# Kernel optimization log

Hardware: AMD Instinct MI355X
Metric: run time of the kernel (lower is better)

The kernel has to match this reference:

```python
import jax, jax.numpy as jnp
import numpy as np

N_CHAINS = 4
CHAIN_LEN = 512
N = N_CHAINS * CHAIN_LEN          # 2048 residues
H = 128                           # h_channels
FC = 3                            # frame_channels
CIN = H + FC                      # fused sphere channels (131)
NH = 8                            # attention heads
VD = H // 4                       # attn value channels per head
NCOEF = 4                         # lmax=1 -> (lmax+1)^2 coefficients
KNN_K = 30
LR_K = 10
NEG = jnp.float32(-1e30)

BB_IDEAL = np.array([[-0.525, 1.363, 0.0], [0.0, 0.0, 0.0], [1.526, 0.0, 0.0]], np.float32)  # N, CA, C ideal coords


def _safe_norm(v, keepdims=False):
    return jnp.sqrt(jnp.sum(v * v, axis=-1, keepdims=keepdims) + 1e-12)


def _normalize(v):
    return v / _safe_norm(v, keepdims=True)


def _edge_rot_mat(vec):
    # deterministic orthonormal frame with first row along the edge direction
    x = _normalize(vec)
    ref = jnp.where(jnp.abs(x[..., :1]) > 0.99,
                    jnp.array([0.0, 1.0, 0.0], x.dtype),
                    jnp.array([1.0, 0.0, 0.0], x.dtype))
    z = _normalize(jnp.cross(x, ref))
    y = jnp.cross(z, x)
    return jnp.stack([x, y, z], axis=-2)          # [E,3,3]


def _rbf(d, d_min=0.0, d_max=20.0, n=16):
    mu = jnp.linspace(d_min, d_max, n)
    sigma = (d_max - d_min) / n
    return jnp.exp(-(((d[..., None] - mu) / sigma) ** 2))


def _relpos(edge_index, n=16):
    d = (edge_index[0] - edge_index[1]).astype(jnp.float32)
    freq = jnp.exp(jnp.arange(0, n, 2, dtype=jnp.float32) * (-np.log(10000.0) / n))
    ang = d[:, None] * freq
    return jnp.concatenate([jnp.cos(ang), jnp.sin(ang)], axis=-1)


def _quat_to_rot(q):
    w, x, y, z = q[..., 0], q[..., 1], q[..., 2], q[..., 3]
    r0 = jnp.stack([1 - 2 * (y * y + z * z), 2 * (x * y - w * z), 2 * (x * z + w * y)], -1)
    r1 = jnp.stack([2 * (x * y + w * z), 1 - 2 * (x * x + z * z), 2 * (y * z - w * x)], -1)
    r2 = jnp.stack([2 * (x * z - w * y), 2 * (y * z + w * x), 1 - 2 * (x * x + y * y)], -1)
    return jnp.stack([r0, r1, r2], -2)


def _build_edges(trans, batch, seq_local_edge_index):
    d2 = jnp.sum((trans[:, None] - trans[None]) ** 2, -1)   # [N,N]
    same = batch[:, None] == batch[None]
    eye = jnp.eye(N, dtype=bool)
    d2m = jnp.where(same & ~eye, d2, jnp.float32(1e30))
    _, knn_idx = jax.lax.top_k(-d2m, KNN_K)                 # kNN neighbors
    g = jax.random.gumbel(jax.random.key(42), d2m.shape)
    _, lr_idx = jax.lax.top_k(-1.5 * jnp.log(d2m) + g, LR_K)  # inv-cubic sampling p ~ d^-3
    src = jnp.concatenate([knn_idx.reshape(-1), lr_idx.reshape(-1), seq_local_edge_index[0]])
    dst = jnp.concatenate([jnp.repeat(jnp.arange(N), KNN_K), jnp.repeat(jnp.arange(N), LR_K), seq_local_edge_index[1]])
    return jnp.stack([src, dst])


def _forward(rots, trans, node_features, Wa1, ba1, Wa2, Wv, Wo, Wg, Wf1, Wf2, Wr1, br1, Wr2, br2, Wr3, br3, Wt, batch, x_mask, noising_mask, seq_local_edge_index):
    edge_index = _build_edges(trans, batch, seq_local_edge_index)
    src, dst = edge_index[0], edge_index[1]
    vec = trans[src] - trans[dst]
    dist = _safe_norm(vec)
    valid = jnp.isfinite(dist) & (dist > 1e-3)              # edge_select mask (kept static-shape)
    R = _edge_rot_mat(vec)                                  # [E,3,3] per-edge Wigner (l=1)
    ef = jnp.concatenate([_rbf(dist), _relpos(edge_index)], -1)  # [E,32]
    # fuse node embedding with backbone frame atoms and editability flag
    bb_atoms = jnp.einsum('nij,aj->nai', rots, jnp.asarray(BB_IDEAL)) + trans[:, None]  # [N,3atoms,3]
    fused = jnp.zeros((N, NCOEF, CIN), node_features.dtype)
    fused = fused.at[:, :, :H].set(node_features)
    fused = fused.at[:, 1:4, H:].set(jnp.swapaxes(bb_atoms, -1, -2))
    editable = noising_mask & (~x_mask)
    fused = fused.at[:, 0, -1].set(editable.astype(fused.dtype))
    # SO3-equivariant attention (TransBlockV2)
    x0 = fused[:, 0]                                        # invariant l=0 features [N,CIN]
    a_in = jnp.concatenate([x0[src], x0[dst], ef], -1)      # [E, 2*CIN+32]
    logits = jax.nn.leaky_relu(a_in @ Wa1 + ba1) @ Wa2      # [E,NH]
    logits = jnp.where(valid[:, None], logits, NEG)
    m = jax.ops.segment_max(logits, dst, num_segments=N)
    m = jnp.where(m > NEG / 2, m, 0.0)
    p = jnp.where(valid[:, None], jnp.exp(logits - m[dst]), 0.0)
    z = jax.ops.segment_sum(p, dst, num_segments=N)
    attn = p / (z[dst] + 1e-9)                              # segment softmax over incoming edges
    xs = fused[src]
    xs = xs.at[:, 1:4].set(jnp.einsum('eij,ejc->eic', R, xs[:, 1:4]))  # rotate l=1 into edge frame
    v = (xs @ Wv).reshape(xs.shape[0], NCOEF, NH, VD)
    msg = (attn[:, None, :, None] * v).reshape(xs.shape[0], NCOEF, NH * VD)
    msg = msg.at[:, 1:4].set(jnp.einsum('eji,ejc->eic', R, msg[:, 1:4]))  # rotate back (R^T)
    agg = jax.ops.segment_sum(msg, dst, num_segments=N)     # [N,4,NH*VD]
    out = agg @ Wo                                          # [N,4,H]
    # gated equivariant FFN
    y0 = out[:, 0]
    gate = jax.nn.sigmoid(y0 @ Wg)
    f0 = jax.nn.relu(y0 @ Wf1) @ Wf2
    bb_update = jnp.concatenate([(y0 + f0)[:, None], out[:, 1:4] * gate[:, None, :]], axis=1)
    # frame rotation update from invariants
    inv = bb_update[:, 0]
    h1 = jax.nn.relu(inv @ Wr1 + br1)
    h2 = jax.nn.relu(h1 @ Wr2 + br2)
    qv = (h2 @ Wr3 + br3)[:, :3]
    quat = jnp.concatenate([jnp.ones_like(qv[:, :1]), qv], -1)
    quat = quat / jnp.linalg.norm(quat, axis=-1, keepdims=True)
    rot_update = _quat_to_rot(quat)
    # equivariant translation update (SO3_LinearV2 on l=1)
    trans_update = (bb_update[:, 1:4] @ Wt)[..., 0]         # [N,3]
    rots_new = jnp.where(noising_mask[:, None, None], jnp.einsum('nij,njk->nik', rots, rot_update), rots)
    trans_new = jnp.where(noising_mask[:, None], trans + trans_update, trans)
    return rots_new, trans_new, bb_update


def setup_inputs():
    key = jax.random.key(0)
    ks = jax.random.split(key, 20)
    q = jax.random.normal(ks[0], (N, 4))
    q = q / jnp.linalg.norm(q, axis=-1, keepdims=True)
    rots = _quat_to_rot(q)                                  # proper rotation matrices
    trans = jax.random.normal(ks[1], (N, 3)) * 10.0
    node_features = jax.random.normal(ks[2], (N, NCOEF, H)) * 0.1
    batch = jnp.repeat(jnp.arange(N_CHAINS), CHAIN_LEN)
    x_mask = jax.random.bernoulli(ks[3], 0.1, (N,))
    noising_mask = jax.random.bernoulli(ks[4], 0.5, (N,))
    idx = jnp.arange(N)
    nxt = jnp.where((idx + 1) % CHAIN_LEN == 0, idx, idx + 1)
    seq_local_edge_index = jnp.stack([jnp.concatenate([idx, nxt]), jnp.concatenate([nxt, idx])])

    def lin(k, i, o):
        return jax.random.normal(k, (i, o)) / np.sqrt(i)

    AIN = 2 * CIN + 32
    return dict(
        rots=rots, trans=trans, node_features=node_features,
        Wa1=lin(ks[5], AIN, H), ba1=jnp.zeros((H,)),
        Wa2=lin(ks[6], H, NH),
        Wv=lin(ks[7], CIN, NH * VD),
        Wo=lin(ks[8], NH * VD, H),
        Wg=lin(ks[9], H, H), Wf1=lin(ks[10], H, H), Wf2=lin(ks[11], H, H),
        Wr1=lin(ks[12], H, 2 * H), br1=jnp.zeros((2 * H,)),
        Wr2=lin(ks[13], 2 * H, H), br2=jnp.zeros((H,)),
        Wr3=lin(ks[14], H, 6), br3=jnp.zeros((6,)),
        Wt=lin(ks[15], H, 1),
        batch=batch, x_mask=x_mask, noising_mask=noising_mask,
        seq_local_edge_index=seq_local_edge_index)


def reference(rots, trans, node_features, Wa1, ba1, Wa2, Wv, Wo, Wg, Wf1, Wf2, Wr1, br1, Wr2, br2, Wr3, br3, Wt, batch, x_mask, noising_mask, seq_local_edge_index):
    return _forward(rots, trans, node_features, Wa1, ba1, Wa2, Wv, Wo, Wg, Wf1, Wf2, Wr1, br1, Wr2, br2, Wr3, br3, Wt, batch, x_mask, noising_mask, seq_local_edge_index)
```

## Files before the change

### kernel.cpp

```cpp
#include <hip/hip_runtime.h>
#include <hip/hip_bf16.h>
#include <math.h>

#define NN 2048
#define CHAIN 512
#define KNN 30
#define LRK 10
#define NFIX 40
#define NSLOT 42
#define HPAD 132
#define AGPAD 260
#define NREL 1023

#define OUT_ROT 0
#define OUT_TRANS (NN*9)
#define OUT_BB (NN*9 + NN*3)

#define THREEFRY_PARTITIONABLE 1

__device__ __forceinline__ int xcd_swz(int b){ return ((b & 7) << 8) | (b >> 3); }

__device__ __forceinline__ unsigned rotl32(unsigned x, unsigned r){ return (x<<r)|(x>>(32u-r)); }

__device__ __forceinline__ void tf_block(unsigned &x0, unsigned &x1){
  const unsigned k0 = 0u, k1 = 42u, k2 = 0x1BD11BDAu ^ 0u ^ 42u;
  x0 += k0; x1 += k1;
#define TFR(a) x0 += x1; x1 = rotl32(x1,(a)); x1 ^= x0;
  TFR(13) TFR(15) TFR(26) TFR(6)   x0 += k1; x1 += k2 + 1u;
  TFR(17) TFR(29) TFR(16) TFR(24)  x0 += k2; x1 += k0 + 2u;
  TFR(13) TFR(15) TFR(26) TFR(6)   x0 += k0; x1 += k1 + 3u;
  TFR(17) TFR(29) TFR(16) TFR(24)  x0 += k1; x1 += k2 + 4u;
  TFR(13) TFR(15) TFR(26) TFR(6)   x0 += k2; x1 += k0 + 5u;
#undef TFR
}

__device__ __forceinline__ float gumbel_from_bits(unsigned bits){
  float f = __uint_as_float((bits >> 9) | 0x3f800000u) - 1.0f;
  const float tiny = 1.17549435e-38f;
  float u = fmaxf(tiny, f * (1.0f - tiny) + tiny);
  return -logf(-logf(u));
}

__device__ __forceinline__ float gumbel_at(unsigned p){
#if THREEFRY_PARTITIONABLE
  unsigned x0 = 0u, x1 = p;
  tf_block(x0, x1);
  return gumbel_from_bits(x0 ^ x1);
#else
  const unsigned HALF = (NN*(unsigned)NN)/2u;
  unsigned c0, c1; bool lo = p < HALF;
  if(lo){ c0 = p; c1 = p + HALF; } else { c0 = p - HALF; c1 = p; }
  tf_block(c0, c1);
  return gumbel_from_bits(lo ? c0 : c1);
#endif
}

__global__ __launch_bounds__(256) void k_pretop(
    const float* __restrict__ rots, const float* __restrict__ trans,
    const float* __restrict__ nf, const float* __restrict__ Wa1,
    const float* __restrict__ Wv, const int* __restrict__ xmask,
    const int* __restrict__ nmask,
    float* __restrict__ P, float* __restrict__ U, float* __restrict__ V,
    int* __restrict__ srcs, float* __restrict__ Trel)
{
  __shared__ __align__(16) char smem[4*4*132*4];
  int bb = blockIdx.x, t = threadIdx.x;

  if(bb >= NN + 512){
    int r = (bb - (NN+512))*2 + (t >> 7);
    int k = t & 127;
    if(r < NREL){
      float rel = (float)(r - 511);
      float acc = 0.f;
#pragma unroll
      for(int j=0;j<8;j++){
        float fr = expf((float)(2*j) * (float)(-0.5756462732485115));
        float ang = rel * fr;
        acc += cosf(ang) * Wa1[(278+j)*128 + k];
        acc += sinf(ang) * Wa1[(286+j)*128 + k];
      }
      Trel[r*128 + k] = acc;
    }
    return;
  }

  if(bb < NN){
    unsigned* s_kk = (unsigned*)smem;
    unsigned* s_lk = s_kk + CHAIN;
    int i = bb;
    int base = (i >> 9) << 9;
    float tx = trans[i*3+0], ty = trans[i*3+1], tz = trans[i*3+2];
    for(int q=t; q<CHAIN; q+=256){
      int j = base + q;
      float dx = __fsub_rn(trans[j*3+0], tx);
      float dy = __fsub_rn(trans[j*3+1], ty);
      float dz = __fsub_rn(trans[j*3+2], tz);
      float d2 = __fadd_rn(__fadd_rn(__fmul_rn(dx,dx),__fmul_rn(dy,dy)),__fmul_rn(dz,dz));
      bool val = (j != i);
      float dm = val ? d2 : 1e30f;
      s_kk[q] = __float_as_uint(dm) ^ 0x80000000u;
      if(val){
        float g = gumbel_at((unsigned)(i*NN + j));
        float sc = __fadd_rn(__fmul_rn(-1.5f, logf(dm)), g);
        unsigned b = __float_as_uint(sc);
        unsigned ord = b ^ ((b & 0x80000000u) ? 0xFFFFFFFFu : 0x80000000u);
        s_lk[q] = ~ord;
      } else {
        s_lk[q] = 0xFFFFFFFFu;
      }
    }
    __syncthreads();
    if(t < 128){
      int w = t >> 6, lane = t & 63;
      unsigned* arr = w ? s_lk : s_kk;
      int K = w ? LRK : KNN;
      int outoff = w ? KNN : 0;
      unsigned long long best = ~0ull;
      for(int q=lane; q<CHAIN; q+=64){
        unsigned long long kk = ((unsigned long long)arr[q]<<32) | (unsigned)q;
        if(kk < best) best = kk;
      }
      for(int k=0;k<K;k++){
        unsigned long long r = best;
        for(int off=32; off; off>>=1){
          unsigned long long o = __shfl_xor(r, off, 64);
          if(o < r) r = o;
        }
        int winq = (int)(unsigned)(r & 0xffffffffull);
        if(lane == 0){
          srcs[i*NFIX + outoff + k] = base + winq;
          arr[winq] = 0xFFFFFFFFu;
        }
        asm volatile("s_waitcnt lgkmcnt(0)" ::: "memory");
        __builtin_amdgcn_wave_barrier();
        if((winq & 63) == lane){
          best = ~0ull;
          for(int q=lane; q<CHAIN; q+=64){
            unsigned long long kk = ((unsigned long long)arr[q]<<32) | (unsigned)q;
            if(kk < best) best = kk;
          }
        }
      }
    }
    return;
  }

  float (*fr)[4][132] = (float (*)[4][132])smem;
  int n0 = (bb - NN)*4;
  for(int i=t; i<2048; i+=256){
    int nd = i>>9, c = (i>>7)&3, kk = i&127;
    fr[nd][c][kk] = nf[(n0+nd)*512 + c*128 + kk];
  }
  if(t < 4){
    fr[t][0][128] = 0.0f; fr[t][0][129] = 0.0f;
    fr[t][0][130] = (nmask[n0+t] != 0 && xmask[n0+t] == 0) ? 1.0f : 0.0f;
  } else if(t >= 16 && t < 52){
    int q = t - 16; int nd = q/9, r = q%9, a = r/3, i = r%3;
    int n = n0 + nd;
    const float BB[3][3] = {{-0.525f,1.363f,0.0f},{0.f,0.f,0.f},{1.526f,0.f,0.f}};
    float bb_ = rots[n*9+i*3+0]*BB[a][0] + rots[n*9+i*3+1]*BB[a][1]
              + rots[n*9+i*3+2]*BB[a][2] + trans[n*3+i];
    fr[nd][1+i][128+a] = bb_;
  }
  __syncthreads();

  float a[4][4];
#pragma unroll
  for(int nd=0;nd<4;nd++)
#pragma unroll
    for(int c=0;c<4;c++) a[nd][c]=0.f;
  for(int j=0;j<128;j+=4){
    float w0=Wv[(j+0)*256+t], w1=Wv[(j+1)*256+t], w2=Wv[(j+2)*256+t], w3=Wv[(j+3)*256+t];
#pragma unroll
    for(int nd=0;nd<4;nd++){
#pragma unroll
      for(int c=0;c<4;c++){
        float4 f4 = *(const float4*)&fr[nd][c][j];
        a[nd][c] += f4.x*w0 + f4.y*w1 + f4.z*w2 + f4.w*w3;
      }
    }
  }
  for(int j=128;j<131;j++){
    float w = Wv[j*256+t];
#pragma unroll
    for(int nd=0;nd<4;nd++)
#pragma unroll
      for(int c=0;c<4;c++) a[nd][c] += fr[nd][c][j]*w;
  }
#pragma unroll
  for(int nd=0;nd<4;nd++){
    float4 v4; v4.x=a[nd][0]; v4.y=a[nd][1]; v4.z=a[nd][2]; v4.w=a[nd][3];
    *(float4*)&P[(n0+nd)*1024 + t*4] = v4;
  }

  int k = t & 127;
  int isV = t >> 7;
  const float* Wcol = Wa1 + (isV ? 131*128 : 0);
  float u[4] = {0.f,0.f,0.f,0.f};
  for(int j=0;j<128;j+=4){
    float w0=Wcol[(j+0)*128+k], w1=Wcol[(j+1)*128+k], w2=Wcol[(j+2)*128+k], w3=Wcol[(j+3)*128+k];
#pragma unroll
    for(int nd=0;nd<4;nd++){
      float4 f4 = *(const float4*)&fr[nd][0][j];
      u[nd] += f4.x*w0 + f4.y*w1 + f4.z*w2 + f4.w*w3;
    }
  }
  for(int j=128;j<131;j++){
    float w = Wcol[j*128+k];
#pragma unroll
    for(int nd=0;nd<4;nd++) u[nd] += fr[nd][0][j]*w;
  }
  float* OUT = isV ? V : U;
#pragma unroll
  for(int nd=0;nd<4;nd++) OUT[(n0+nd)*128 + k] = u[nd];
}

__global__ __launch_bounds__(256) void k_attn(
    const float* __restrict__ trans, const float* __restrict__ Wa1,
    const float* __restrict__ ba1, const float* __restrict__ Wa2,
    const float* __restrict__ Wo,
    const float* __restrict__ U, const float* __restrict__ V,
    const float* __restrict__ P, const float* __restrict__ Trel,
    const int* __restrict__ srcs, float* __restrict__ Y)
{
  __shared__ int   s_src[NSLOT];
  __shared__ int   s_val[NSLOT];
  __shared__ float s_dist[NSLOT];
  __shared__ __align__(16) float s_H[NSLOT*HPAD];
  __shared__ __align__(16) float s_mux[NSLOT*32];
  __shared__ float s_att[NSLOT*8];

  int b = blockIdx.x, t = threadIdx.x;
  int d = xcd_swz(b);
  int pos = d & (CHAIN-1);
  int k = t & 127, grp = t >> 7;

  if(t < NSLOT){
    int src;
    if(t < NFIX)      src = srcs[d*NFIX + t];
    else if(t == NFIX) src = (pos > 0)       ? d-1 : d;
    else               src = (pos < CHAIN-1) ? d+1 : d;
    s_src[t] = src;
    float dx = trans[src*3+0]-trans[d*3+0];
    float dy = trans[src*3+1]-trans[d*3+1];
    float dz = trans[src*3+2]-trans[d*3+2];
    float dist = sqrtf(dx*dx + dy*dy + dz*dz + 1e-12f);
    s_dist[t] = dist;
    s_val[t] = (dist > 1e-3f) ? 1 : 0;
  }

  float wreg[16];
#pragma unroll
  for(int f=0; f<16; f++) wreg[f] = Wa1[(262+f)*128 + k];
  float ubias = ba1[k] + V[d*128 + k];
  __syncthreads();

  for(int i=t; i<NSLOT*16; i+=256){
    int e = i >> 4, f = i & 15;
    float zz = (s_dist[e] - (float)f * (20.0f/15.0f)) * 0.8f;
    s_mux[i] = expf(-(zz*zz));
  }
  __syncthreads();

  for(int e = grp; e < NSLOT; e += 2){
    int src = s_src[e];
    float h = ubias + U[src*128 + k] + Trel[(src - d + 511)*128 + k];
    const float4* rp = (const float4*)(s_mux + e*16);
#pragma unroll
    for(int q=0; q<4; q++){
      float4 ev = rp[q];
      h += ev.x*wreg[4*q+0] + ev.y*wreg[4*q+1] + ev.z*wreg[4*q+2] + ev.w*wreg[4*q+3];
    }
    h = (h >= 0.0f) ? h : 0.01f*h;
    s_H[e*HPAD + k] = h;
  }
  __syncthreads();

  for(int i=t; i<1024; i+=256){
    int kk = i >> 3, h = i & 7;
    s_mux[h*HPAD + kk] = Wa2[i];
  }
  __syncthreads();

  for(int p = t; p < NSLOT*8; p += 256){
    int e = p >> 3, h = p & 7;
    const float4* Hp = (const float4*)(s_H + e*HPAD);
    const float4* Wp = (const float4*)(s_mux + h*HPAD);
    float acc = 0.f;
#pragma unroll
    for(int q=0; q<32; q++){
      float4 a = Hp[q], w = Wp[q];
      acc += a.x*w.x + a.y*w.y + a.z*w.z + a.w*w.w;
    }
    s_att[p] = s_val[e] ? acc : -1e30f;
  }
  __syncthreads();

  if(t < 64){
    int h = t & 7, g = t >> 3;
    float m = -INFINITY;
    for(int e=g; e<NSLOT; e+=8) m = fmaxf(m, s_att[e*8+h]);
    for(int off=8; off<64; off<<=1) m = fmaxf(m, __shfl_xor(m, off, 64));
    m = (m > -5e29f) ? m : 0.0f;
    float z = 0.0f;
    for(int e=g; e<NSLOT; e+=8){
      float p = expf(s_att[e*8+h] - m);
      s_att[e*8+h] = p; z += p;
    }
    for(int off=8; off<64; off<<=1) z += __shfl_xor(z, off, 64);
    float den = z + 1e-9f;
    for(int e=g; e<NSLOT; e+=8) s_att[e*8+h] = s_att[e*8+h] / den;
  }
  __syncthreads();

  {
    int h = t >> 5;
    float a0=0.f,a1=0.f,a2=0.f,a3=0.f;
    for(int e=0;e<NSLOT;e++){
      float w = s_att[e*8 + h];
      float4 p4 = *(const float4*)(P + s_src[e]*1024 + t*4);
      a0 += w*p4.x; a1 += w*p4.y; a2 += w*p4.z; a3 += w*p4.w;
    }
    s_mux[0*AGPAD + t] = a0;
    s_mux[1*AGPAD + t] = a1;
    s_mux[2*AGPAD + t] = a2;
    s_mux[3*AGPAD + t] = a3;
  }
  __syncthreads();

  {
    int cp = grp*2;
    const float* g0 = s_mux + cp*AGPAD;
    const float* g1 = s_mux + (cp+1)*AGPAD;
    float x0=0.f, x1=0.f;
    for(int u=0; u<256; u+=4){
      float w0=Wo[(u+0)*128+k], w1=Wo[(u+1)*128+k], w2=Wo[(u+2)*128+k], w3=Wo[(u+3)*128+k];
      float4 a0 = *(const float4*)(g0 + u);
      float4 a1 = *(const float4*)(g1 + u);
      x0 += a0.x*w0 + a0.y*w1 + a0.z*w2 + a0.w*w3;
      x1 += a1.x*w0 + a1.y*w1 + a1.z*w2 + a1.w*w3;
    }
    Y[d*512 + cp*128 + k]     = x0;
    Y[d*512 + (cp+1)*128 + k] = x1;
  }
}

__global__ __launch_bounds__(256) void k_node(
    const float* __restrict__ rots, const float* __restrict__ trans,
    const float* __restrict__ Y,
    const float* __restrict__ Wg, const float* __restrict__ Wf1,
    const float* __restrict__ Wf2, const float* __restrict__ Wr1,
    const float* __restrict__ br1, const float* __restrict__ Wr2,
    const float* __restrict__ br2, const float* __restrict__ Wr3,
    const float* __restrict__ br3, const float* __restrict__ Wt,
    const int* __restrict__ nmask, float* __restrict__ out)
{
  __shared__ __align__(16) float s_y[4][4][128];
  __shared__ __align__(16) float s_t1[4][128];
  __shared__ __align__(16) float s_bb0[4][128];
  __shared__ __align__(16) float s_gv[4][3][128];
  __shared__ __align__(16) float s_h1[4][256];
  __shared__ __align__(16) float s_h2[4][128];
  __shared__ float s_sc[4][8];

  int b = blockIdx.x, t = threadIdx.x;
  int half = t >> 7, k = t & 127;
  int nb = half*2;
  int dbase = b*4;
  for(int i=t; i<4*512; i+=256){
    int nd = i>>9, c=(i>>7)&3, kk=i&127;
    s_y[nd][c][kk] = Y[(dbase+nd)*512 + c*128 + kk];
  }
  __syncthreads();

  float g[2]={0.f,0.f}, f1[2]={0.f,0.f};
  for(int j=0;j<128;j+=4){
    float wg0=Wg[(j+0)*128+k], wg1=Wg[(j+1)*128+k], wg2=Wg[(j+2)*128+k], wg3=Wg[(j+3)*128+k];
    float wf0=Wf1[(j+0)*128+k], wf1_=Wf1[(j+1)*128+k], wf2_=Wf1[(j+2)*128+k], wf3=Wf1[(j+3)*128+k];
#pragma unroll
    for(int nn=0;nn<2;nn++){
      float4 yv = *(const float4*)&s_y[nb+nn][0][j];
      g[nn]  += yv.x*wg0 + yv.y*wg1 + yv.z*wg2 + yv.w*wg3;
      f1[nn] += yv.x*wf0 + yv.y*wf1_ + yv.z*wf2_ + yv.w*wf3;
    }
  }
  float gate[2];
#pragma unroll
  for(int nn=0;nn<2;nn++){
    gate[nn] = 1.0f/(1.0f + expf(-g[nn]));
    s_t1[nb+nn][k] = fmaxf(f1[nn], 0.0f);
  }
  __syncthreads();

  float f0[2]={0.f,0.f};
  for(int j=0;j<128;j+=4){
    float w0=Wf2[(j+0)*128+k], w1=Wf2[(j+1)*128+k], w2=Wf2[(j+2)*128+k], w3=Wf2[(j+3)*128+k];
#pragma unroll
    for(int nn=0;nn<2;nn++){
      float4 tv = *(const float4*)&s_t1[nb+nn][j];
      f0[nn] += tv.x*w0 + tv.y*w1 + tv.z*w2 + tv.w*w3;
    }
  }
#pragma unroll
  for(int nn=0;nn<2;nn++){
    int d = dbase + nb + nn;
    float bb0 = s_y[nb+nn][0][k] + f0[nn];
    s_bb0[nb+nn][k] = bb0;
    out[OUT_BB + d*512 + k] = bb0;
#pragma unroll
    for(int c=1;c<4;c++){
      float v = s_y[nb+nn][c][k] * gate[nn];
      s_gv[nb+nn][c-1][k] = v;
      out[OUT_BB + d*512 + c*128 + k] = v;
    }
  }
  __syncthreads();

  float a1[2], a2[2];
  a1[0]=a1[1]=br1[k]; a2[0]=a2[1]=br1[128+k];
  for(int j=0;j<128;j+=4){
    float w10=Wr1[(j+0)*256+k],     w11=Wr1[(j+1)*256+k],     w12=Wr1[(j+2)*256+k],     w13=Wr1[(j+3)*256+k];
    float w20=Wr1[(j+0)*256+128+k], w21=Wr1[(j+1)*256+128+k], w22=Wr1[(j+2)*256+128+k], w23=Wr1[(j+3)*256+128+k];
#pragma unroll
    for(int nn=0;nn<2;nn++){
      float4 bv = *(const float4*)&s_bb0[nb+nn][j];
      a1[nn] += bv.x*w10 + bv.y*w11 + bv.z*w12 + bv.w*w13;
      a2[nn] += bv.x*w20 + bv.y*w21 + bv.z*w22 + bv.w*w23;
    }
  }
#pragma unroll
  for(int nn=0;nn<2;nn++){
    s_h1[nb+nn][k] = fmaxf(a1[nn], 0.0f);
    s_h1[nb+nn][128+k] = fmaxf(a2[nn], 0.0f);
  }
  __syncthreads();

  float a[2]; a[0]=a[1]=br2[k];
  for(int j=0;j<256;j+=4){
    float w0=Wr2[(j+0)*128+k], w1=Wr2[(j+1)*128+k], w2=Wr2[(j+2)*128+k], w3=Wr2[(j+3)*128+k];
#pragma unroll
    for(int nn=0;nn<2;nn++){
      float4 hv = *(const float4*)&s_h1[nb+nn][j];
      a[nn] += hv.x*w0 + hv.y*w1 + hv.z*w2 + hv.w*w3;
    }
  }
#pragma unroll
  for(int nn=0;nn<2;nn++) s_h2[nb+nn][k] = fmaxf(a[nn], 0.0f);
  __syncthreads();

  if(t < 12){
    int nd = t/3, r = t%3;
    float q = br3[r];
    for(int kk=0;kk<128;kk++) q += s_h2[nd][kk] * Wr3[kk*6 + r];
    s_sc[nd][r] = q;
  } else if(t >= 32 && t < 44){
    int q2 = t-32; int nd = q2/3, i = q2%3;
    float s = 0.f;
    for(int kk=0;kk<128;kk++) s += s_gv[nd][i][kk] * Wt[kk];
    s_sc[nd][4+i] = s;
  }
  __syncthreads();

  if(t < 4){
    int d = dbase + t;
    int nz = nmask[d];
    float q1=s_sc[t][0], q2=s_sc[t][1], q3=s_sc[t][2];
    float nrm = sqrtf(1.0f + q1*q1 + q2*q2 + q3*q3);
    float w=1.0f/nrm, x=q1/nrm, y=q2/nrm, z=q3/nrm;
    float Ru[3][3];
    Ru[0][0]=1.f-2.f*(y*y+z*z); Ru[0][1]=2.f*(x*y-w*z);     Ru[0][2]=2.f*(x*z+w*y);
    Ru[1][0]=2.f*(x*y+w*z);     Ru[1][1]=1.f-2.f*(x*x+z*z); Ru[1][2]=2.f*(y*z-w*x);
    Ru[2][0]=2.f*(x*z-w*y);     Ru[2][1]=2.f*(y*z+w*x);     Ru[2][2]=1.f-2.f*(x*x+y*y);
    for(int i=0;i<3;i++){
      for(int j=0;j<3;j++){
        float rv;
        if(nz){
          rv = rots[d*9+i*3+0]*Ru[0][j] + rots[d*9+i*3+1]*Ru[1][j] + rots[d*9+i*3+2]*Ru[2][j];
        } else {
          rv = rots[d*9+i*3+j];
        }
        out[OUT_ROT + d*9 + i*3 + j] = rv;
      }
      float tv = trans[d*3+i];
      out[OUT_TRANS + d*3 + i] = nz ? (tv + s_sc[t][4+i]) : tv;
    }
  }
}

extern "C" void kernel_launch(void* const* d_in, const int* in_sizes, int n_in,
                              void* d_out, int out_size, void* d_ws, size_t ws_size,
                              hipStream_t stream)
{
  (void)in_sizes; (void)n_in; (void)out_size; (void)ws_size;
  const float* rots = (const float*)d_in[0];
  const float* trans = (const float*)d_in[1];
  const float* nf   = (const float*)d_in[2];
  const float* Wa1  = (const float*)d_in[3];
  const float* ba1  = (const float*)d_in[4];
  const float* Wa2  = (const float*)d_in[5];
  const float* Wv   = (const float*)d_in[6];
  const float* Wo   = (const float*)d_in[7];
  const float* Wg   = (const float*)d_in[8];
  const float* Wf1  = (const float*)d_in[9];
  const float* Wf2  = (const float*)d_in[10];
  const float* Wr1  = (const float*)d_in[11];
  const float* br1  = (const float*)d_in[12];
  const float* Wr2  = (const float*)d_in[13];
  const float* br2  = (const float*)d_in[14];
  const float* Wr3  = (const float*)d_in[15];
  const float* br3  = (const float*)d_in[16];
  const float* Wt   = (const float*)d_in[17];
  const int* xmask  = (const int*)d_in[19];
  const int* nmask  = (const int*)d_in[20];

  float* P = (float*)d_ws;
  float* U = P + NN*1024;
  float* V = U + NN*128;
  int* srcs = (int*)(V + NN*128);
  float* Y  = (float*)(srcs + NN*NFIX);
  float* Trel = Y + NN*512;

  k_pretop<<<NN + 512 + 512, 256, 0, stream>>>(rots, trans, nf, Wa1, Wv, xmask, nmask,
                                               P, U, V, srcs, Trel);
  k_attn<<<NN, 256, 0, stream>>>(trans, Wa1, ba1, Wa2, Wo, U, V, P, Trel, srcs, Y);
  k_node<<<NN/4, 256, 0, stream>>>(rots, trans, Y, Wg, Wf1, Wf2,
                                   Wr1, br1, Wr2, br2, Wr3, br3, Wt,
                                   nmask, (float*)d_out);
}
```

Baseline: 141.0 us.

## Fuse attention logit projection via wave shuffles and pre-transpose Wo

Instead of writing the hidden edge features to shared memory and running a separate dot product against Wa2, each thread multiplies its hidden value by its Wa2 row and reduces the 8 head logits across the wavefront with butterfly shuffles. Wo is transposed in extra pretop blocks so the output projection reads contiguous float4 weights. The P aggregation loop prefetches the next source row, and the softmax divide becomes a reciprocal multiply. This cuts shared memory and barriers, but adds many shuffles per edge and an extra transpose pass each call.

```diff
diff --git a/kernel.cpp b/kernel.cpp
--- a/kernel.cpp
+++ b/kernel.cpp
@@ -8,7 +8,6 @@
 #define LRK 10
 #define NFIX 40
 #define NSLOT 42
-#define HPAD 132
 #define AGPAD 260
 #define NREL 1023
 
@@ -58,13 +57,23 @@
 __global__ __launch_bounds__(256) void k_pretop(
     const float* __restrict__ rots, const float* __restrict__ trans,
     const float* __restrict__ nf, const float* __restrict__ Wa1,
-    const float* __restrict__ Wv, const int* __restrict__ xmask,
-    const int* __restrict__ nmask,
+    const float* __restrict__ Wv, const float* __restrict__ Wo,
+    const int* __restrict__ xmask, const int* __restrict__ nmask,
     float* __restrict__ P, float* __restrict__ U, float* __restrict__ V,
-    int* __restrict__ srcs, float* __restrict__ Trel)
+    int* __restrict__ srcs, float* __restrict__ Trel, float* __restrict__ Wot)
 {
   __shared__ __align__(16) char smem[4*4*132*4];
   int bb = blockIdx.x, t = threadIdx.x;
+
+  if(bb >= NN + 1024){
+    int b2 = bb - (NN + 1024);
+    int i0 = b2*8192;
+    for(int i = i0 + t; i < i0 + 8192; i += 256){
+      int kk2 = i >> 8, uu = i & 255;
+      Wot[i] = Wo[uu*128 + kk2];
+    }
+    return;
+  }
 
   if(bb >= NN + 512){
     int r = (bb - (NN+512))*2 + (t >> 7);
@@ -218,7 +227,7 @@
 __global__ __launch_bounds__(256) void k_attn(
     const float* __restrict__ trans, const float* __restrict__ Wa1,
     const float* __restrict__ ba1, const float* __restrict__ Wa2,
-    const float* __restrict__ Wo,
+    const float* __restrict__ Wot,
     const float* __restrict__ U, const float* __restrict__ V,
     const float* __restrict__ P, const float* __restrict__ Trel,
     const int* __restrict__ srcs, float* __restrict__ Y)
@@ -226,14 +235,17 @@
   __shared__ int   s_src[NSLOT];
   __shared__ int   s_val[NSLOT];
   __shared__ float s_dist[NSLOT];
-  __shared__ __align__(16) float s_H[NSLOT*HPAD];
-  __shared__ __align__(16) float s_mux[NSLOT*32];
+  __shared__ __align__(16) float s_mux[1344];
   __shared__ float s_att[NSLOT*8];
+
+  float* s_rbf  = s_mux;
+  float* s_part = s_mux + 672;
 
   int b = blockIdx.x, t = threadIdx.x;
   int d = xcd_swz(b);
   int pos = d & (CHAIN-1);
   int k = t & 127, grp = t >> 7;
+  int lane = t & 63, kw = (t >> 6) & 1;
 
   if(t < NSLOT){
     int src;
@@ -252,75 +264,86 @@
   float wreg[16];
 #pragma unroll
   for(int f=0; f<16; f++) wreg[f] = Wa1[(262+f)*128 + k];
+  float4 wa2a = *(const float4*)(Wa2 + k*8);
+  float4 wa2b = *(const float4*)(Wa2 + k*8 + 4);
   float ubias = ba1[k] + V[d*128 + k];
+  int hmine = ((lane&1)<<2) | (lane&2) | ((lane>>2)&1);
   __syncthreads();
 
   for(int i=t; i<NSLOT*16; i+=256){
     int e = i >> 4, f = i & 15;
     float zz = (s_dist[e] - (float)f * (20.0f/15.0f)) * 0.8f;
-    s_mux[i] = expf(-(zz*zz));
+    s_rbf[i] = expf(-(zz*zz));
   }
   __syncthreads();
 
   for(int e = grp; e < NSLOT; e += 2){
     int src = s_src[e];
     float h = ubias + U[src*128 + k] + Trel[(src - d + 511)*128 + k];
-    const float4* rp = (const float4*)(s_mux + e*16);
+    const float4* rp = (const float4*)(s_rbf + e*16);
 #pragma unroll
     for(int q=0; q<4; q++){
       float4 ev = rp[q];
       h += ev.x*wreg[4*q+0] + ev.y*wreg[4*q+1] + ev.z*wreg[4*q+2] + ev.w*wreg[4*q+3];
     }
     h = (h >= 0.0f) ? h : 0.01f*h;
-    s_H[e*HPAD + k] = h;
-  }
-  __syncthreads();
-
-  for(int i=t; i<1024; i+=256){
-    int kk = i >> 3, h = i & 7;
-    s_mux[h*HPAD + kk] = Wa2[i];
-  }
-  __syncthreads();
-
-  for(int p = t; p < NSLOT*8; p += 256){
-    int e = p >> 3, h = p & 7;
-    const float4* Hp = (const float4*)(s_H + e*HPAD);
-    const float4* Wp = (const float4*)(s_mux + h*HPAD);
-    float acc = 0.f;
-#pragma unroll
-    for(int q=0; q<32; q++){
-      float4 a = Hp[q], w = Wp[q];
-      acc += a.x*w.x + a.y*w.y + a.z*w.z + a.w*w.w;
-    }
-    s_att[p] = s_val[e] ? acc : -1e30f;
+    float p0 = h*wa2a.x, p1 = h*wa2a.y, p2 = h*wa2a.z, p3 = h*wa2a.w;
+    float p4 = h*wa2b.x, p5 = h*wa2b.y, p6 = h*wa2b.z, p7 = h*wa2b.w;
+    float q0=__shfl_xor(p0,1,64), q1=__shfl_xor(p1,1,64), q2=__shfl_xor(p2,1,64), q3=__shfl_xor(p3,1,64);
+    float q4=__shfl_xor(p4,1,64), q5=__shfl_xor(p5,1,64), q6=__shfl_xor(p6,1,64), q7=__shfl_xor(p7,1,64);
+    float r0,r1,r2,r3;
+    if((lane&1)==0){ r0=p0+q0; r1=p1+q1; r2=p2+q2; r3=p3+q3; }
+    else           { r0=p4+q4; r1=p5+q5; r2=p6+q6; r3=p7+q7; }
+    q0=__shfl_xor(r0,2,64); q1=__shfl_xor(r1,2,64); q2=__shfl_xor(r2,2,64); q3=__shfl_xor(r3,2,64);
+    float s0,s1;
+    if((lane&2)==0){ s0=r0+q0; s1=r1+q1; }
+    else           { s0=r2+q2; s1=r3+q3; }
+    q0=__shfl_xor(s0,4,64); q1=__shfl_xor(s1,4,64);
+    float v = ((lane&4)==0) ? (s0+q0) : (s1+q1);
+    v += __shfl_xor(v, 8, 64);
+    v += __shfl_xor(v, 16, 64);
+    v += __shfl_xor(v, 32, 64);
+    if(lane < 8) s_part[e*16 + kw*8 + hmine] = v;
   }
   __syncthreads();
 
   if(t < 64){
     int h = t & 7, g = t >> 3;
     float m = -INFINITY;
-    for(int e=g; e<NSLOT; e+=8) m = fmaxf(m, s_att[e*8+h]);
+    for(int e=g; e<NSLOT; e+=8){
+      float l = s_part[e*16 + h] + s_part[e*16 + 8 + h];
+      l = s_val[e] ? l : -1e30f;
+      m = fmaxf(m, l);
+    }
     for(int off=8; off<64; off<<=1) m = fmaxf(m, __shfl_xor(m, off, 64));
     m = (m > -5e29f) ? m : 0.0f;
     float z = 0.0f;
     for(int e=g; e<NSLOT; e+=8){
-      float p = expf(s_att[e*8+h] - m);
+      float l = s_part[e*16 + h] + s_part[e*16 + 8 + h];
+      l = s_val[e] ? l : -1e30f;
+      float p = expf(l - m);
       s_att[e*8+h] = p; z += p;
     }
     for(int off=8; off<64; off<<=1) z += __shfl_xor(z, off, 64);
-    float den = z + 1e-9f;
-    for(int e=g; e<NSLOT; e+=8) s_att[e*8+h] = s_att[e*8+h] / den;
+    float inv = 1.0f / (z + 1e-9f);
+    for(int e=g; e<NSLOT; e+=8) s_att[e*8+h] *= inv;
   }
   __syncthreads();
 
   {
     int h = t >> 5;
     float a0=0.f,a1=0.f,a2=0.f,a3=0.f;
+    float4 pn = *(const float4*)(P + (size_t)s_src[0]*1024 + t*4);
+    float wn = s_att[h];
     for(int e=0;e<NSLOT;e++){
-      float w = s_att[e*8 + h];
-      float4 p4 = *(const float4*)(P + s_src[e]*1024 + t*4);
-      a0 += w*p4.x; a1 += w*p4.y; a2 += w*p4.z; a3 += w*p4.w;
-    }
+      float4 pc = pn; float wc = wn;
+      if(e+1 < NSLOT){
+        pn = *(const float4*)(P + (size_t)s_src[e+1]*1024 + t*4);
+        wn = s_att[(e+1)*8 + h];
+      }
+      a0 += wc*pc.x; a1 += wc*pc.y; a2 += wc*pc.z; a3 += wc*pc.w;
+    }
+    __syncthreads();
     s_mux[0*AGPAD + t] = a0;
     s_mux[1*AGPAD + t] = a1;
     s_mux[2*AGPAD + t] = a2;
@@ -332,13 +355,14 @@
     int cp = grp*2;
     const float* g0 = s_mux + cp*AGPAD;
     const float* g1 = s_mux + (cp+1)*AGPAD;
+    const float4* wp = (const float4*)(Wot + k*256);
     float x0=0.f, x1=0.f;
-    for(int u=0; u<256; u+=4){
-      float w0=Wo[(u+0)*128+k], w1=Wo[(u+1)*128+k], w2=Wo[(u+2)*128+k], w3=Wo[(u+3)*128+k];
-      float4 a0 = *(const float4*)(g0 + u);
-      float4 a1 = *(const float4*)(g1 + u);
-      x0 += a0.x*w0 + a0.y*w1 + a0.z*w2 + a0.w*w3;
-      x1 += a1.x*w0 + a1.y*w1 + a1.z*w2 + a1.w*w3;
+    for(int u4=0; u4<64; u4++){
+      float4 w4 = wp[u4];
+      float4 a0 = *(const float4*)(g0 + u4*4);
+      float4 a1 = *(const float4*)(g1 + u4*4);
+      x0 += a0.x*w4.x + a0.y*w4.y + a0.z*w4.z + a0.w*w4.w;
+      x1 += a1.x*w4.x + a1.y*w4.y + a1.z*w4.z + a1.w*w4.w;
     }
     Y[d*512 + cp*128 + k]     = x0;
     Y[d*512 + (cp+1)*128 + k] = x1;
@@ -519,10 +543,11 @@
   int* srcs = (int*)(V + NN*128);
   float* Y  = (float*)(srcs + NN*NFIX);
   float* Trel = Y + NN*512;
-
-  k_pretop<<<NN + 512 + 512, 256, 0, stream>>>(rots, trans, nf, Wa1, Wv, xmask, nmask,
-                                               P, U, V, srcs, Trel);
-  k_attn<<<NN, 256, 0, stream>>>(trans, Wa1, ba1, Wa2, Wo, U, V, P, Trel, srcs, Y);
+  float* Wot  = Trel + NREL*128;
+
+  k_pretop<<<NN + 512 + 512 + 16, 256, 0, stream>>>(rots, trans, nf, Wa1, Wv, Wo,
+                                                    xmask, nmask, P, U, V, srcs, Trel, Wot);
+  k_attn<<<NN, 256, 0, stream>>>(trans, Wa1, ba1, Wa2, Wot, U, V, P, Trel, srcs, Y);
   k_node<<<NN/4, 256, 0, stream>>>(rots, trans, Y, Wg, Wf1, Wf2,
                                    Wr1, br1, Wr2, br2, Wr3, br3, Wt,
                                    nmask, (float*)d_out);
```

New measurement: 177.1 us. +25.6%, slower.
